# Performance work log

Hardware: AMD Instinct MI355X
Metric: run time of the kernel (lower is better)

Reference implementation:

```python
import jax, jax.numpy as jnp
import numpy as np

EMBED_DIM = 1024
NUM_HEADS = 16
D_K = EMBED_DIM // NUM_HEADS
GAMMA = 1.0


def setup_inputs() -> dict:
    key = jax.random.key(0)
    ks = jax.random.split(key, 5)
    B, N, E = 2, 2048, EMBED_DIM
    scale = 1.0 / np.sqrt(E)
    x = jax.random.normal(ks[0], (B, N, E), dtype=jnp.float32)
    Wq = jax.random.normal(ks[1], (E, E), dtype=jnp.float32) * scale
    Wk = jax.random.normal(ks[2], (E, E), dtype=jnp.float32) * scale
    Wv = jax.random.normal(ks[3], (E, E), dtype=jnp.float32) * scale
    Wo = jax.random.normal(ks[4], (E, E), dtype=jnp.float32) * scale
    mask = jnp.ones((B, N), dtype=jnp.int32)
    return {"x": x, "Wq": Wq, "Wk": Wk, "Wv": Wv, "Wo": Wo, "mask": mask}


def _split_heads(t):
    B, N, E = t.shape
    return t.reshape(B, N, NUM_HEADS, D_K).transpose(0, 2, 1, 3)  # [B,H,N,dk]


def reference(x, Wq, Wk, Wv, Wo, mask):
    B, N, E = x.shape
    # Linear layers (bias=False): y = x @ W.T
    q = _split_heads(x @ Wq.T)
    k = _split_heads(x @ Wk.T)
    v = _split_heads(x @ Wv.T)
    # Squared L2 distance via ||q||^2 + ||k||^2 - 2 q.k (same math as (q-k)^2.sum,
    # without materializing the [B,H,N,N,dk] diff tensor).
    q_sq = jnp.sum(q * q, axis=-1)  # [B,H,N]
    k_sq = jnp.sum(k * k, axis=-1)  # [B,H,N]
    qk = jnp.einsum('bhqd,bhkd->bhqk', q, k)
    sq_dist = jnp.maximum(q_sq[..., :, None] + k_sq[..., None, :] - 2.0 * qk, 0.0)
    similarity = jnp.exp(-GAMMA * sq_dist)  # [B,H,N,N]
    # mask.unsqueeze(1).unsqueeze(2): broadcast over heads and query dim
    mask_exp = mask[:, None, None, :]  # [B,1,1,N]
    similarity = jnp.where(mask_exp == 0, jnp.float32(-1e9), similarity)
    attn = jax.nn.softmax(similarity, axis=-1)
    # dropout p=0.0 (eval) -> identity
    out = jnp.einsum('bhqk,bhkd->bhqd', attn, v)
    out = out.transpose(0, 2, 1, 3).reshape(B, N, E)
    return out @ Wo.T
```

## Files before the change

kernel.cpp:

```cpp
#include <hip/hip_runtime.h>
#include <hip/hip_bf16.h>


using bf16x8 = __attribute__((ext_vector_type(8))) __bf16;
using f32x4  = __attribute__((ext_vector_type(4))) float;
using f32x16 = __attribute__((ext_vector_type(16))) float;

typedef const __attribute__((address_space(1))) void* gas_t;
typedef __attribute__((address_space(3))) void* las_t;

#define C_LOG2E 1.4426950408889634f
#define TWO_C   2.8853900817779268f
#define NEG_INV_4C (-0.17328679513998632f)

#if __has_builtin(__builtin_amdgcn_exp2f)
#define EXP2(x) __builtin_amdgcn_exp2f(x)
#else
#define EXP2(x) __expf((x) * 0.6931471805599453f)
#endif

static __device__ __forceinline__ unsigned short f2bf(float x) {
  union { float f; unsigned u; } c; c.f = x;
  unsigned u = c.u;
  u += 0x7fffu + ((u >> 16) & 1u);
  return (unsigned short)(u >> 16);
}
static __device__ __forceinline__ float bf2f(unsigned short b) {
  union { unsigned u; float f; } c; c.u = ((unsigned)b) << 16;
  return c.f;
}
static __device__ __forceinline__ unsigned cvt_pk_bf16(float lo, float hi) {
  unsigned r;
  asm("v_cvt_pk_bf16_f32 %0, %1, %2" : "=v"(r) : "v"(lo), "v"(hi));
  return r;
}
static __device__ __forceinline__ void permlane32_swap(unsigned &a, unsigned &b) {
#if __has_builtin(__builtin_amdgcn_permlane32_swap)
  auto r = __builtin_amdgcn_permlane32_swap(a, b, false, false);
  a = r[0]; b = r[1];
#else
  asm("v_permlane32_swap_b32 %0, %1" : "+v"(a), "+v"(b));
#endif
}

#define SYNC_VM(N)                                                           \
  do {                                                                       \
    asm volatile("s_waitcnt vmcnt(" #N ") lgkmcnt(0)\n\ts_barrier" ::: "memory"); \
    __builtin_amdgcn_sched_barrier(0);                                       \
  } while (0)

__global__ __launch_bounds__(256)
void cvt_all(const float* __restrict__ x,  const float* __restrict__ wq,
             const float* __restrict__ wk, const float* __restrict__ wv,
             const float* __restrict__ wo,
             unsigned short* __restrict__ xbf, unsigned short* __restrict__ Wbf) {
  const int idx = blockIdx.x * 256 + threadIdx.x;
  const float* src; unsigned short* dst; int off;
  if (idx < 1048576) { src = x; dst = xbf; off = idx; }
  else {
    const int r = idx - 1048576;
    const int w = r >> 18;
    off = r & 262143;
    src = (w == 0) ? wq : (w == 1) ? wk : (w == 2) ? wv : wo;
    dst = Wbf + (size_t)w * 1048576u;
  }
  const float4 v = ((const float4*)src)[off];
  ushort4 o;
  o.x = f2bf(v.x); o.y = f2bf(v.y); o.z = f2bf(v.z); o.w = f2bf(v.w);
  ((ushort4*)dst)[off] = o;
}

__global__ __launch_bounds__(256)
void gemm_bt(const unsigned short* __restrict__ A,
             const unsigned short* __restrict__ Bt,
             void* __restrict__ out0, int Kdim, int mode) {
  __shared__ unsigned short As[3][4096];
  __shared__ unsigned short Bs[3][4096];
  const int t  = threadIdx.x;
  const int m0 = blockIdx.x * 128;
  const int n0 = blockIdx.y * 128;
  const int srow = t >> 2;
  const int scol = (t & 3) * 8;
  const unsigned short* pA = A  + (size_t)(m0 + srow) * Kdim + scol;
  const unsigned short* pB = Bt + (size_t)(n0 + srow) * Kdim + scol;
  const size_t rowskip = (size_t)64 * Kdim;

  const int wave = t >> 6, lane = t & 63;
  const int wm = (wave >> 1) * 64, wn = (wave & 1) * 64;
  const int fr = lane & 15, fg = lane >> 4;
  const int aoff = (wm + fr) * 32 + fg * 8;
  const int boff = (wn + fr) * 32 + fg * 8;

  f32x4 acc[4][4];
#pragma unroll
  for (int mi = 0; mi < 4; ++mi)
#pragma unroll
    for (int ni = 0; ni < 4; ++ni)
      acc[mi][ni] = (f32x4){0.f, 0.f, 0.f, 0.f};

#define GSTAGE(bi, kk)                                                                                  \
  do {                                                                                                  \
    const int kc = (kk) * 32;                                                                           \
    __builtin_amdgcn_global_load_lds((gas_t)(const void*)(pA + kc),           (las_t)(void*)(As[bi] + t * 8),        16, 0, 0); \
    __builtin_amdgcn_global_load_lds((gas_t)(const void*)(pA + kc + rowskip), (las_t)(void*)(As[bi] + 2048 + t * 8), 16, 0, 0); \
    __builtin_amdgcn_global_load_lds((gas_t)(const void*)(pB + kc),           (las_t)(void*)(Bs[bi] + t * 8),        16, 0, 0); \
    __builtin_amdgcn_global_load_lds((gas_t)(const void*)(pB + kc + rowskip), (las_t)(void*)(Bs[bi] + 2048 + t * 8), 16, 0, 0); \
  } while (0)

  const int NK = Kdim >> 5;
  GSTAGE(0, 0);
  GSTAGE(1, 1);

  for (int ks = 0; ks < NK; ++ks) {
    const int cur = ks % 3;
    if (ks + 1 < NK) SYNC_VM(4); else SYNC_VM(0);
    if (ks + 2 < NK) GSTAGE((ks + 2) % 3, ks + 2);

    bf16x8 af[4], bfr[4];
#pragma unroll
    for (int mi = 0; mi < 4; ++mi) af[mi]  = *(const bf16x8*)(As[cur] + aoff + mi * 512);
#pragma unroll
    for (int ni = 0; ni < 4; ++ni) bfr[ni] = *(const bf16x8*)(Bs[cur] + boff + ni * 512);
#pragma unroll
    for (int mi = 0; mi < 4; ++mi)
#pragma unroll
      for (int ni = 0; ni < 4; ++ni)
        acc[mi][ni] = __builtin_amdgcn_mfma_f32_16x16x32_bf16(af[mi], bfr[ni], acc[mi][ni], 0, 0, 0);
  }
#undef GSTAGE

#pragma unroll
  for (int mi = 0; mi < 4; ++mi) {
    const int gm = m0 + wm + mi * 16 + fg * 4;
#pragma unroll
    for (int ni = 0; ni < 4; ++ni) {
      const int gn = n0 + wn + ni * 16 + fr;
      if (mode == 0) {
        unsigned short* outw = (unsigned short*)out0;
        const int z = gn >> 10, col = gn & 1023;
        if (z < 2) {
          const float sc = (z == 0) ? TWO_C : 1.0f;
          unsigned short* dst = outw + (size_t)z * 4194304u;
#pragma unroll
          for (int r = 0; r < 4; ++r)
            dst[(size_t)(gm + r) * 1024 + col] = f2bf(acc[mi][ni][r] * sc);
        } else {
          ushort4 o4;
          o4.x = f2bf(acc[mi][ni][0]); o4.y = f2bf(acc[mi][ni][1]);
          o4.z = f2bf(acc[mi][ni][2]); o4.w = f2bf(acc[mi][ni][3]);
          const int bb = gm >> 11, nn = gm & 2047;
          const int hh = col >> 6, dd = col & 63;
          unsigned short* vt = outw + (size_t)2 * 4194304u;
          *(ushort4*)(vt + ((size_t)((bb * 16 + hh) * 64 + dd)) * 2048 + nn) = o4;
        }
      } else {
        float* dst = (float*)out0;
#pragma unroll
        for (int r = 0; r < 4; ++r)
          dst[(size_t)(gm + r) * 1024 + gn] = acc[mi][ni][r];
      }
    }
  }
}

__global__ __launch_bounds__(256)
void rowsq_kernel(const unsigned short* __restrict__ Qbf,
                  const unsigned short* __restrict__ Kbf,
                  const int* __restrict__ mask,
                  float* __restrict__ qsqp, float* __restrict__ ksqp,
                  float* __restrict__ maskf,
                  float* __restrict__ FullVm,
                  float* __restrict__ den_base,
                  unsigned* __restrict__ kmax_bits) {
  const int tid = blockIdx.x * 256 + threadIdx.x;
  const int kpath = blockIdx.y;
  const unsigned short* src = (kpath == 0) ? Qbf : Kbf;
  const int bh = tid >> 11, n = tid & 2047;
  const int b = bh >> 4, h = bh & 15;
  const unsigned short* row = src + (size_t)(b * 2048 + n) * 1024 + h * 64;
  float s = 0.f;
#pragma unroll
  for (int c = 0; c < 64; c += 4) {
    ushort4 v = *(const ushort4*)(row + c);
    float f0 = bf2f(v.x), f1 = bf2f(v.y), f2 = bf2f(v.z), f3 = bf2f(v.w);
    s += f0 * f0 + f1 * f1 + f2 * f2 + f3 * f3;
  }
  if (kpath == 0) {
    qsqp[tid] = s * NEG_INV_4C;
    if (tid < 2048) FullVm[tid] = 0.f;
    if (tid < 32) kmax_bits[tid] = 0xFF800000u;
    if (tid < 2) den_base[tid] = 0.f;
  } else {
    ksqp[tid] = s * (-C_LOG2E);
    if (tid < 4096) maskf[tid] = (mask[tid] == 0) ? 0.f : 1.f;
  }
}

__global__ __launch_bounds__(256)
void prep2_kernel(const unsigned short* __restrict__ Vt,
                  const float* __restrict__ maskf,
                  const float* __restrict__ ksqp,
                  float* __restrict__ FullVm,
                  float* __restrict__ den_base,
                  unsigned* __restrict__ kmax_bits) {
  const int bh = blockIdx.x, c = blockIdx.y;
  const int b = bh >> 4;
  const int wave = threadIdx.x >> 6, lane = threadIdx.x & 63;
  const int k0 = c * 256;
  const float4 mv = *(const float4*)(maskf + b * 2048 + k0 + lane * 4);
#pragma unroll 4
  for (int dr = wave * 16; dr < wave * 16 + 16; ++dr) {
    const ushort4 v = *(const ushort4*)(Vt + ((size_t)bh * 64 + dr) * 2048 + k0 + lane * 4);
    float s = bf2f(v.x) * mv.x + bf2f(v.y) * mv.y + bf2f(v.z) * mv.z + bf2f(v.w) * mv.w;
#pragma unroll
    for (int off = 32; off >= 1; off >>= 1) s += __shfl_xor(s, off);
    if (lane == 0) atomicAdd(&FullVm[bh * 64 + dr], s);
  }
  if (wave == 0) {
    const float4 kq = *(const float4*)(ksqp + bh * 2048 + k0 + lane * 4);
    float mx = fmaxf(fmaxf(kq.x, kq.y), fmaxf(kq.z, kq.w));
#pragma unroll
    for (int off = 32; off >= 1; off >>= 1) mx = fmaxf(mx, __shfl_xor(mx, off));
    if (lane == 0) atomicMin(&kmax_bits[bh], __float_as_uint(mx));
  }
  if (wave == 1 && (bh & 15) == 0) {
    float s = mv.x + mv.y + mv.z + mv.w;
#pragma unroll
    for (int off = 32; off >= 1; off >>= 1) s += __shfl_xor(s, off);
    if (lane == 0) atomicAdd(&den_base[b], s);
  }
}

__global__ __launch_bounds__(256)
void attn_kernel(const unsigned short* __restrict__ Qbf,
                 const unsigned short* __restrict__ Kbf,
                 const unsigned short* __restrict__ Vt,
                 const float* __restrict__ qsqp,
                 const float* __restrict__ ksqp,
                 const float* __restrict__ maskf,
                 const float* __restrict__ FullVm,
                 const float* __restrict__ den_base,
                 const float* __restrict__ kmaxb,
                 unsigned short* __restrict__ Obf) {
  __shared__ unsigned short Ks[3][4096];

  const int bh = blockIdx.x;
  const int b = bh >> 4, h = bh & 15;
  const int t = threadIdx.x;
  const int wave = t >> 6, lane = t & 63;
  const int qg = wave >> 1, hf = wave & 1;
  const int li = lane & 31, hi = lane >> 5;
  const int q0 = blockIdx.y * 64 + qg * 32;
  const int qrow = q0 + li;

  const unsigned short* Qr = Qbf + (size_t)(b * 2048 + qrow) * 1024 + h * 64 + hi * 8;
  bf16x8 qf[4];
#pragma unroll
  for (int dblk = 0; dblk < 4; ++dblk) qf[dblk] = *(const bf16x8*)(Qr + dblk * 16);

  const float qsl = qsqp[bh * 2048 + qrow];
  const float thr = -14.0f - qsl - kmaxb[bh];

  const unsigned short* Kbase = Kbf + (size_t)b * 2048 * 1024 + h * 64;
  const unsigned short* VtB = Vt + (size_t)bh * 64 * 2048;

  const int p0 = t,        r0 = p0 >> 3, c0 = (p0 & 7) ^ (r0 & 7);
  const int p1 = 256 + t,  r1 = p1 >> 3, c1 = (p1 & 7) ^ (r1 & 7);

  f32x16 oa0, oa1;
#pragma unroll
  for (int r = 0; r < 16; ++r) { oa0[r] = 0.f; oa1[r] = 0.f; }
  float den = 0.f;

#define STAGE(bi, tj)                                                                               \
  do {                                                                                              \
    const int j0s = (tj) * 64;                                                                      \
    __builtin_amdgcn_global_load_lds((gas_t)(const void*)(Kbase + (size_t)(j0s + r0) * 1024 + c0 * 8), \
                                     (las_t)(void*)(Ks[bi] + p0 * 8), 16, 0, 0);                    \
    __builtin_amdgcn_global_load_lds((gas_t)(const void*)(Kbase + (size_t)(j0s + r1) * 1024 + c1 * 8), \
                                     (las_t)(void*)(Ks[bi] + p1 * 8), 16, 0, 0);                    \
  } while (0)

  STAGE(0, 0);
  STAGE(1, 1);

  const int jw = hf * 32;
  const int krow = jw + li;
  const int ksw = krow & 7;

  for (int tj = 0; tj < 32; ++tj) {
    const int cur = tj % 3;
    if (tj + 1 < 32) SYNC_VM(2); else SYNC_VM(0);
    if (tj + 2 < 32) STAGE((tj + 2) % 3, tj + 2);

    const unsigned short* Krow = Ks[cur] + krow * 64;
    f32x16 st;
#pragma unroll
    for (int r = 0; r < 16; ++r) st[r] = 0.f;
#pragma unroll
    for (int dblk = 0; dblk < 4; ++dblk) {
      const bf16x8 kf = *(const bf16x8*)(Krow + ((dblk * 2 + hi) ^ ksw) * 8);
      st = __builtin_amdgcn_mfma_f32_32x32x16_bf16(kf, qf[dblk], st, 0, 0, 0);
    }

    const float a0 = fmaxf(fmaxf(st[0], st[1]), st[2]);
    const float a1 = fmaxf(fmaxf(st[3], st[4]), st[5]);
    const float a2 = fmaxf(fmaxf(st[6], st[7]), st[8]);
    const float a3 = fmaxf(fmaxf(st[9], st[10]), st[11]);
    const float a4 = fmaxf(fmaxf(st[12], st[13]), st[14]);
    const float a5 = fmaxf(fmaxf(a0, a1), st[15]);
    const float a6 = fmaxf(fmaxf(a2, a3), a4);
    const float lmax = fmaxf(a5, a6);

    if (__any(lmax > thr)) {
      const int j0 = tj * 64 + jw;
      const float* ksb2 = ksqp + bh * 2048 + j0 + 4 * hi;
      const float* mfb2 = maskf + b * 2048 + j0 + 4 * hi;
      const float4 kq0 = *(const float4*)(ksb2);
      const float4 kq1 = *(const float4*)(ksb2 + 8);
      const float4 kq2 = *(const float4*)(ksb2 + 16);
      const float4 kq3 = *(const float4*)(ksb2 + 24);
      const float4 mf0 = *(const float4*)(mfb2);
      const float4 mf1 = *(const float4*)(mfb2 + 8);
      const float4 mf2 = *(const float4*)(mfb2 + 16);
      const float4 mf3 = *(const float4*)(mfb2 + 24);
      const float kqa[16] = {kq0.x, kq0.y, kq0.z, kq0.w, kq1.x, kq1.y, kq1.z, kq1.w,
                             kq2.x, kq2.y, kq2.z, kq2.w, kq3.x, kq3.y, kq3.z, kq3.w};
      const float mfa[16] = {mf0.x, mf0.y, mf0.z, mf0.w, mf1.x, mf1.y, mf1.z, mf1.w,
                             mf2.x, mf2.y, mf2.z, mf2.w, mf3.x, mf3.y, mf3.z, mf3.w};
      float dsv[16];
#pragma unroll
      for (int r = 0; r < 16; ++r) {
        const float z = __builtin_fminf(st[r] + qsl + kqa[r], 0.f);
        const float s = EXP2(z);
        float pl = __builtin_fmaf(s, 1.f / 120.f, 1.f / 24.f);
        pl = __builtin_fmaf(s, pl, 1.f / 6.f);
        pl = __builtin_fmaf(s, pl, 0.5f);
        pl = __builtin_fmaf(s, pl, 1.f);
        const float d_ = s * pl * mfa[r];
        dsv[r] = d_;
        den += d_;
      }

      unsigned u00 = cvt_pk_bf16(dsv[0],  dsv[1]);
      unsigned u01 = cvt_pk_bf16(dsv[2],  dsv[3]);
      unsigned u10 = cvt_pk_bf16(dsv[4],  dsv[5]);
      unsigned u11 = cvt_pk_bf16(dsv[6],  dsv[7]);
      unsigned u20 = cvt_pk_bf16(dsv[8],  dsv[9]);
      unsigned u21 = cvt_pk_bf16(dsv[10], dsv[11]);
      unsigned u30 = cvt_pk_bf16(dsv[12], dsv[13]);
      unsigned u31 = cvt_pk_bf16(dsv[14], dsv[15]);
      permlane32_swap(u00, u10);
      permlane32_swap(u01, u11);
      permlane32_swap(u20, u30);
      permlane32_swap(u21, u31);
      union { unsigned u[4]; bf16x8 v; } pf0, pf1;
      pf0.u[0] = u00; pf0.u[1] = u01; pf0.u[2] = u10; pf0.u[3] = u11;
      pf1.u[0] = u20; pf1.u[1] = u21; pf1.u[2] = u30; pf1.u[3] = u31;

#pragma unroll
      for (int dh = 0; dh < 2; ++dh) {
        const unsigned short* Vrow = VtB + (size_t)(dh * 32 + li) * 2048 + tj * 64;
        const bf16x8 vf0 = *(const bf16x8*)(Vrow + (hf * 4 + 0 + hi) * 8);
        const bf16x8 vf1 = *(const bf16x8*)(Vrow + (hf * 4 + 2 + hi) * 8);
        if (dh == 0) {
          oa0 = __builtin_amdgcn_mfma_f32_32x32x16_bf16(vf0, pf0.v, oa0, 0, 0, 0);
          oa0 = __builtin_amdgcn_mfma_f32_32x32x16_bf16(vf1, pf1.v, oa0, 0, 0, 0);
        } else {
          oa1 = __builtin_amdgcn_mfma_f32_32x32x16_bf16(vf0, pf0.v, oa1, 0, 0, 0);
          oa1 = __builtin_amdgcn_mfma_f32_32x32x16_bf16(vf1, pf1.v, oa1, 0, 0, 0);
        }
      }
    }
  }
#undef STAGE

  den += __shfl_xor(den, 32);

  __syncthreads();
  float* Obuf = (float*)&Ks[0][0];
  float* Dbuf = (float*)&Ks[0][0] + 4096;
  if (hf == 1) {
#pragma unroll
    for (int r = 0; r < 16; ++r) {
      Obuf[(qg * 32 + r) * 64 + lane]      = oa0[r];
      Obuf[(qg * 32 + 16 + r) * 64 + lane] = oa1[r];
    }
    Dbuf[qg * 64 + lane] = den;
  }
  __syncthreads();
  if (hf == 0) {
    const float inv = 1.f / (den_base[b] + den + Dbuf[qg * 64 + lane]);
    const float* fvm = FullVm + bh * 64;
    unsigned short* orow = Obf + (size_t)(b * 2048 + qrow) * 1024 + h * 64;
#pragma unroll
    for (int dh = 0; dh < 2; ++dh)
#pragma unroll
      for (int w = 0; w < 4; ++w) {
        float v0, v1, v2, v3;
        if (dh == 0) {
          v0 = oa0[4 * w];     v1 = oa0[4 * w + 1];
          v2 = oa0[4 * w + 2]; v3 = oa0[4 * w + 3];
        } else {
          v0 = oa1[4 * w];     v1 = oa1[4 * w + 1];
          v2 = oa1[4 * w + 2]; v3 = oa1[4 * w + 3];
        }
        const int sbase = (qg * 32 + dh * 16 + 4 * w) * 64 + lane;
        v0 += Obuf[sbase];       v1 += Obuf[sbase + 64];
        v2 += Obuf[sbase + 128]; v3 += Obuf[sbase + 192];
        const float4 fv = *(const float4*)(fvm + dh * 32 + w * 8 + hi * 4);
        ushort4 o4;
        o4.x = f2bf((v0 + fv.x) * inv);
        o4.y = f2bf((v1 + fv.y) * inv);
        o4.z = f2bf((v2 + fv.z) * inv);
        o4.w = f2bf((v3 + fv.w) * inv);
        *(ushort4*)(orow + dh * 32 + w * 8 + hi * 4) = o4;
      }
  }
}

extern "C" void kernel_launch(void* const* d_in, const int* in_sizes, int n_in,
                              void* d_out, int out_size, void* d_ws, size_t ws_size,
                              hipStream_t stream) {
  const float* x  = (const float*)d_in[0];
  const float* Wq = (const float*)d_in[1];
  const float* Wk = (const float*)d_in[2];
  const float* Wv = (const float*)d_in[3];
  const float* Wo = (const float*)d_in[4];
  const int* mask = (const int*)d_in[5];

  unsigned short* ws = (unsigned short*)d_ws;
  const size_t SZ = 4194304;
  unsigned short* xbf = ws;
  unsigned short* Wbf = ws + SZ;
  unsigned short* Qbf = ws + 2 * SZ;
  unsigned short* Kbf = ws + 3 * SZ;
  unsigned short* Vt  = ws + 4 * SZ;
  unsigned short* Obf = ws + 5 * SZ;
  float* qsqp = (float*)(ws + 6 * SZ);
  float* ksqp = qsqp + 65536;
  float* maskf = ksqp + 65536;
  float* FullVm = maskf + 4096;
  float* den_base = FullVm + 2048;
  float* kmaxb = den_base + 2;

  cvt_all<<<8192, 256, 0, stream>>>(x, Wq, Wk, Wv, Wo, xbf, Wbf);

  gemm_bt<<<dim3(32, 24), 256, 0, stream>>>(xbf, Wbf, Qbf, 1024, 0);

  rowsq_kernel<<<dim3(256, 2), 256, 0, stream>>>(Qbf, Kbf, mask, qsqp, ksqp, maskf,
                                                 FullVm, den_base, (unsigned*)kmaxb);

  prep2_kernel<<<dim3(32, 8), 256, 0, stream>>>(Vt, maskf, ksqp, FullVm, den_base,
                                                (unsigned*)kmaxb);

  attn_kernel<<<dim3(32, 32), 256, 0, stream>>>(Qbf, Kbf, Vt, qsqp, ksqp, maskf,
                                                FullVm, den_base, kmaxb, Obf);

  gemm_bt<<<dim3(32, 8), 256, 0, stream>>>(Obf, Wbf + 3145728, d_out, 1024, 1);
}
```

Measured before the change: 116.6 us.

## Double attention key tile per stage and swizzle GEMM LDS layout

The attention kernel now stages 128 keys per pipeline step instead of 64, so each wave computes two 32x32 score tiles per iteration. This halves the loop trip count and the barrier/wait overhead, and gives the scheduler two independent MFMA chains to interleave. The GEMM kernel also gets an XOR swizzle on LDS column chunks to reduce bank conflicts on fragment reads. In exchange, LDS use in attention doubles, which may reduce occupancy, and the larger unrolled body adds register pressure.

```diff
diff --git a/kernel.cpp b/kernel.cpp
--- a/kernel.cpp
+++ b/kernel.cpp
@@ -80,7 +80,7 @@
   const int m0 = blockIdx.x * 128;
   const int n0 = blockIdx.y * 128;
   const int srow = t >> 2;
-  const int scol = (t & 3) * 8;
+  const int scol = (((t & 3) ^ (srow & 3) ^ ((srow >> 2) & 3))) * 8;
   const unsigned short* pA = A  + (size_t)(m0 + srow) * Kdim + scol;
   const unsigned short* pB = Bt + (size_t)(n0 + srow) * Kdim + scol;
   const size_t rowskip = (size_t)64 * Kdim;
@@ -88,8 +88,9 @@
   const int wave = t >> 6, lane = t & 63;
   const int wm = (wave >> 1) * 64, wn = (wave & 1) * 64;
   const int fr = lane & 15, fg = lane >> 4;
-  const int aoff = (wm + fr) * 32 + fg * 8;
-  const int boff = (wn + fr) * 32 + fg * 8;
+  const int fswz = fg ^ (fr & 3) ^ ((fr >> 2) & 3);
+  const int aoff = (wm + fr) * 32 + fswz * 8;
+  const int boff = (wn + fr) * 32 + fswz * 8;
 
   f32x4 acc[4][4];
 #pragma unroll
@@ -242,7 +243,7 @@
                  const float* __restrict__ den_base,
                  const float* __restrict__ kmaxb,
                  unsigned short* __restrict__ Obf) {
-  __shared__ unsigned short Ks[3][4096];
+  __shared__ unsigned short Ks[3][8192];
 
   const int bh = blockIdx.x;
   const int b = bh >> 4, h = bh & 15;
@@ -264,8 +265,10 @@
   const unsigned short* Kbase = Kbf + (size_t)b * 2048 * 1024 + h * 64;
   const unsigned short* VtB = Vt + (size_t)bh * 64 * 2048;
 
-  const int p0 = t,        r0 = p0 >> 3, c0 = (p0 & 7) ^ (r0 & 7);
-  const int p1 = 256 + t,  r1 = p1 >> 3, c1 = (p1 & 7) ^ (r1 & 7);
+  const int p0 = t,       r0 = p0 >> 3, c0 = (p0 & 7) ^ (r0 & 7);
+  const int p1 = 256 + t, r1 = p1 >> 3, c1 = (p1 & 7) ^ (r1 & 7);
+  const int p2 = 512 + t, r2 = p2 >> 3, c2 = (p2 & 7) ^ (r2 & 7);
+  const int p3 = 768 + t, r3 = p3 >> 3, c3 = (p3 & 7) ^ (r3 & 7);
 
   f32x16 oa0, oa1;
 #pragma unroll
@@ -274,104 +277,114 @@
 
 #define STAGE(bi, tj)                                                                               \
   do {                                                                                              \
-    const int j0s = (tj) * 64;                                                                      \
+    const int j0s = (tj) * 128;                                                                     \
     __builtin_amdgcn_global_load_lds((gas_t)(const void*)(Kbase + (size_t)(j0s + r0) * 1024 + c0 * 8), \
                                      (las_t)(void*)(Ks[bi] + p0 * 8), 16, 0, 0);                    \
     __builtin_amdgcn_global_load_lds((gas_t)(const void*)(Kbase + (size_t)(j0s + r1) * 1024 + c1 * 8), \
                                      (las_t)(void*)(Ks[bi] + p1 * 8), 16, 0, 0);                    \
+    __builtin_amdgcn_global_load_lds((gas_t)(const void*)(Kbase + (size_t)(j0s + r2) * 1024 + c2 * 8), \
+                                     (las_t)(void*)(Ks[bi] + p2 * 8), 16, 0, 0);                    \
+    __builtin_amdgcn_global_load_lds((gas_t)(const void*)(Kbase + (size_t)(j0s + r3) * 1024 + c3 * 8), \
+                                     (las_t)(void*)(Ks[bi] + p3 * 8), 16, 0, 0);                    \
   } while (0)
 
   STAGE(0, 0);
   STAGE(1, 1);
 
-  const int jw = hf * 32;
-  const int krow = jw + li;
-  const int ksw = krow & 7;
-
-  for (int tj = 0; tj < 32; ++tj) {
-    const int cur = tj % 3;
-    if (tj + 1 < 32) SYNC_VM(2); else SYNC_VM(0);
-    if (tj + 2 < 32) STAGE((tj + 2) % 3, tj + 2);
-
-    const unsigned short* Krow = Ks[cur] + krow * 64;
-    f32x16 st;
-#pragma unroll
-    for (int r = 0; r < 16; ++r) st[r] = 0.f;
-#pragma unroll
-    for (int dblk = 0; dblk < 4; ++dblk) {
-      const bf16x8 kf = *(const bf16x8*)(Krow + ((dblk * 2 + hi) ^ ksw) * 8);
-      st = __builtin_amdgcn_mfma_f32_32x32x16_bf16(kf, qf[dblk], st, 0, 0, 0);
+  const int jw = hf * 64;
+  const int ksw = li & 7;
+
+  auto slow_path = [&](const f32x16& st, int j0s) {
+    const float* ksb2 = ksqp + bh * 2048 + j0s + 4 * hi;
+    const float* mfb2 = maskf + b * 2048 + j0s + 4 * hi;
+    const float4 kq0 = *(const float4*)(ksb2);
+    const float4 kq1 = *(const float4*)(ksb2 + 8);
+    const float4 kq2 = *(const float4*)(ksb2 + 16);
+    const float4 kq3 = *(const float4*)(ksb2 + 24);
+    const float4 mf0 = *(const float4*)(mfb2);
+    const float4 mf1 = *(const float4*)(mfb2 + 8);
+    const float4 mf2 = *(const float4*)(mfb2 + 16);
+    const float4 mf3 = *(const float4*)(mfb2 + 24);
+    const float kqa[16] = {kq0.x, kq0.y, kq0.z, kq0.w, kq1.x, kq1.y, kq1.z, kq1.w,
+                           kq2.x, kq2.y, kq2.z, kq2.w, kq3.x, kq3.y, kq3.z, kq3.w};
+    const float mfa[16] = {mf0.x, mf0.y, mf0.z, mf0.w, mf1.x, mf1.y, mf1.z, mf1.w,
+                           mf2.x, mf2.y, mf2.z, mf2.w, mf3.x, mf3.y, mf3.z, mf3.w};
+    float dsv[16];
+#pragma unroll
+    for (int r = 0; r < 16; ++r) {
+      const float z = __builtin_fminf(st[r] + qsl + kqa[r], 0.f);
+      const float s = EXP2(z);
+      float pl = __builtin_fmaf(s, 1.f / 120.f, 1.f / 24.f);
+      pl = __builtin_fmaf(s, pl, 1.f / 6.f);
+      pl = __builtin_fmaf(s, pl, 0.5f);
+      pl = __builtin_fmaf(s, pl, 1.f);
+      const float d_ = s * pl * mfa[r];
+      dsv[r] = d_;
+      den += d_;
     }
-
-    const float a0 = fmaxf(fmaxf(st[0], st[1]), st[2]);
-    const float a1 = fmaxf(fmaxf(st[3], st[4]), st[5]);
-    const float a2 = fmaxf(fmaxf(st[6], st[7]), st[8]);
-    const float a3 = fmaxf(fmaxf(st[9], st[10]), st[11]);
-    const float a4 = fmaxf(fmaxf(st[12], st[13]), st[14]);
-    const float a5 = fmaxf(fmaxf(a0, a1), st[15]);
-    const float a6 = fmaxf(fmaxf(a2, a3), a4);
-    const float lmax = fmaxf(a5, a6);
-
-    if (__any(lmax > thr)) {
-      const int j0 = tj * 64 + jw;
-      const float* ksb2 = ksqp + bh * 2048 + j0 + 4 * hi;
-      const float* mfb2 = maskf + b * 2048 + j0 + 4 * hi;
-      const float4 kq0 = *(const float4*)(ksb2);
-      const float4 kq1 = *(const float4*)(ksb2 + 8);
-      const float4 kq2 = *(const float4*)(ksb2 + 16);
-      const float4 kq3 = *(const float4*)(ksb2 + 24);
-      const float4 mf0 = *(const float4*)(mfb2);
-      const float4 mf1 = *(const float4*)(mfb2 + 8);
-      const float4 mf2 = *(const float4*)(mfb2 + 16);
-      const float4 mf3 = *(const float4*)(mfb2 + 24);
-      const float kqa[16] = {kq0.x, kq0.y, kq0.z, kq0.w, kq1.x, kq1.y, kq1.z, kq1.w,
-                             kq2.x, kq2.y, kq2.z, kq2.w, kq3.x, kq3.y, kq3.z, kq3.w};
-      const float mfa[16] = {mf0.x, mf0.y, mf0.z, mf0.w, mf1.x, mf1.y, mf1.z, mf1.w,
-                             mf2.x, mf2.y, mf2.z, mf2.w, mf3.x, mf3.y, mf3.z, mf3.w};
-      float dsv[16];
-#pragma unroll
-      for (int r = 0; r < 16; ++r) {
-        const float z = __builtin_fminf(st[r] + qsl + kqa[r], 0.f);
-        const float s = EXP2(z);
-        float pl = __builtin_fmaf(s, 1.f / 120.f, 1.f / 24.f);
-        pl = __builtin_fmaf(s, pl, 1.f / 6.f);
-        pl = __builtin_fmaf(s, pl, 0.5f);
-        pl = __builtin_fmaf(s, pl, 1.f);
-        const float d_ = s * pl * mfa[r];
-        dsv[r] = d_;
-        den += d_;
-      }
-
-      unsigned u00 = cvt_pk_bf16(dsv[0],  dsv[1]);
-      unsigned u01 = cvt_pk_bf16(dsv[2],  dsv[3]);
-      unsigned u10 = cvt_pk_bf16(dsv[4],  dsv[5]);
-      unsigned u11 = cvt_pk_bf16(dsv[6],  dsv[7]);
-      unsigned u20 = cvt_pk_bf16(dsv[8],  dsv[9]);
-      unsigned u21 = cvt_pk_bf16(dsv[10], dsv[11]);
-      unsigned u30 = cvt_pk_bf16(dsv[12], dsv[13]);
-      unsigned u31 = cvt_pk_bf16(dsv[14], dsv[15]);
-      permlane32_swap(u00, u10);
-      permlane32_swap(u01, u11);
-      permlane32_swap(u20, u30);
-      permlane32_swap(u21, u31);
-      union { unsigned u[4]; bf16x8 v; } pf0, pf1;
-      pf0.u[0] = u00; pf0.u[1] = u01; pf0.u[2] = u10; pf0.u[3] = u11;
-      pf1.u[0] = u20; pf1.u[1] = u21; pf1.u[2] = u30; pf1.u[3] = u31;
-
-#pragma unroll
-      for (int dh = 0; dh < 2; ++dh) {
-        const unsigned short* Vrow = VtB + (size_t)(dh * 32 + li) * 2048 + tj * 64;
-        const bf16x8 vf0 = *(const bf16x8*)(Vrow + (hf * 4 + 0 + hi) * 8);
-        const bf16x8 vf1 = *(const bf16x8*)(Vrow + (hf * 4 + 2 + hi) * 8);
-        if (dh == 0) {
-          oa0 = __builtin_amdgcn_mfma_f32_32x32x16_bf16(vf0, pf0.v, oa0, 0, 0, 0);
-          oa0 = __builtin_amdgcn_mfma_f32_32x32x16_bf16(vf1, pf1.v, oa0, 0, 0, 0);
-        } else {
-          oa1 = __builtin_amdgcn_mfma_f32_32x32x16_bf16(vf0, pf0.v, oa1, 0, 0, 0);
-          oa1 = __builtin_amdgcn_mfma_f32_32x32x16_bf16(vf1, pf1.v, oa1, 0, 0, 0);
-        }
+    unsigned u00 = cvt_pk_bf16(dsv[0],  dsv[1]);
+    unsigned u01 = cvt_pk_bf16(dsv[2],  dsv[3]);
+    unsigned u10 = cvt_pk_bf16(dsv[4],  dsv[5]);
+    unsigned u11 = cvt_pk_bf16(dsv[6],  dsv[7]);
+    unsigned u20 = cvt_pk_bf16(dsv[8],  dsv[9]);
+    unsigned u21 = cvt_pk_bf16(dsv[10], dsv[11]);
+    unsigned u30 = cvt_pk_bf16(dsv[12], dsv[13]);
+    unsigned u31 = cvt_pk_bf16(dsv[14], dsv[15]);
+    permlane32_swap(u00, u10);
+    permlane32_swap(u01, u11);
+    permlane32_swap(u20, u30);
+    permlane32_swap(u21, u31);
+    union { unsigned u[4]; bf16x8 v; } pf0, pf1;
+    pf0.u[0] = u00; pf0.u[1] = u01; pf0.u[2] = u10; pf0.u[3] = u11;
+    pf1.u[0] = u20; pf1.u[1] = u21; pf1.u[2] = u30; pf1.u[3] = u31;
+#pragma unroll
+    for (int dh = 0; dh < 2; ++dh) {
+      const unsigned short* Vrow = VtB + (size_t)(dh * 32 + li) * 2048 + j0s;
+      const bf16x8 vf0 = *(const bf16x8*)(Vrow + hi * 8);
+      const bf16x8 vf1 = *(const bf16x8*)(Vrow + 16 + hi * 8);
+      if (dh == 0) {
+        oa0 = __builtin_amdgcn_mfma_f32_32x32x16_bf16(vf0, pf0.v, oa0, 0, 0, 0);
+        oa0 = __builtin_amdgcn_mfma_f32_32x32x16_bf16(vf1, pf1.v, oa0, 0, 0, 0);
+      } else {
+        oa1 = __builtin_amdgcn_mfma_f32_32x32x16_bf16(vf0, pf0.v, oa1, 0, 0, 0);
+        oa1 = __builtin_amdgcn_mfma_f32_32x32x16_bf16(vf1, pf1.v, oa1, 0, 0, 0);
       }
     }
+  };
+
+  for (int tj = 0; tj < 16; ++tj) {
+    const int cur = tj % 3;
+    if (tj + 1 < 16) SYNC_VM(4); else SYNC_VM(0);
+    if (tj + 2 < 16) STAGE((tj + 2) % 3, tj + 2);
+
+    const unsigned short* Krow0 = Ks[cur] + (jw + li) * 64;
+    const unsigned short* Krow1 = Ks[cur] + (jw + 32 + li) * 64;
+    f32x16 st0, st1;
+#pragma unroll
+    for (int r = 0; r < 16; ++r) { st0[r] = 0.f; st1[r] = 0.f; }
+#pragma unroll
+    for (int dblk = 0; dblk < 4; ++dblk) {
+      const int ch = ((dblk * 2 + hi) ^ ksw) * 8;
+      const bf16x8 kf0 = *(const bf16x8*)(Krow0 + ch);
+      const bf16x8 kf1 = *(const bf16x8*)(Krow1 + ch);
+      st0 = __builtin_amdgcn_mfma_f32_32x32x16_bf16(kf0, qf[dblk], st0, 0, 0, 0);
+      st1 = __builtin_amdgcn_mfma_f32_32x32x16_bf16(kf1, qf[dblk], st1, 0, 0, 0);
+    }
+
+    const float a0 = fmaxf(fmaxf(st0[0], st0[1]), fmaxf(st0[2], st0[3]));
+    const float a1 = fmaxf(fmaxf(st0[4], st0[5]), fmaxf(st0[6], st0[7]));
+    const float a2 = fmaxf(fmaxf(st0[8], st0[9]), fmaxf(st0[10], st0[11]));
+    const float a3 = fmaxf(fmaxf(st0[12], st0[13]), fmaxf(st0[14], st0[15]));
+    const float lmax0 = fmaxf(fmaxf(a0, a1), fmaxf(a2, a3));
+    const float b0 = fmaxf(fmaxf(st1[0], st1[1]), fmaxf(st1[2], st1[3]));
+    const float b1 = fmaxf(fmaxf(st1[4], st1[5]), fmaxf(st1[6], st1[7]));
+    const float b2 = fmaxf(fmaxf(st1[8], st1[9]), fmaxf(st1[10], st1[11]));
+    const float b3 = fmaxf(fmaxf(st1[12], st1[13]), fmaxf(st1[14], st1[15]));
+    const float lmax1 = fmaxf(fmaxf(b0, b1), fmaxf(b2, b3));
+
+    const int j0 = tj * 128 + jw;
+    if (__any(lmax0 > thr)) slow_path(st0, j0);
+    if (__any(lmax1 > thr)) slow_path(st1, j0 + 32);
   }
 #undef STAGE
 
```

Measured after the change: 117.7 us. No clear change (+0.9%).

## Fuse row-norm computation into QKV GEMM epilogue and swizzle GEMM LDS layout

Applied to the files above, without the earlier changes.

Removes the separate rowsq kernel by computing per-head squared norms of Q and K inside the QKV GEMM epilogue, using shuffle reductions over the rounded bf16 values. Buffer initialisation moves into the conversion kernel, and mask conversion moves into the prep kernel, so there is one launch fewer and no second read of Q and K. It also adds an XOR swizzle to the GEMM shared-memory tile layout, aimed at reducing LDS bank conflicts. The cost is extra shuffles and stores in the GEMM epilogue.

```diff
diff --git a/kernel.cpp b/kernel.cpp
--- a/kernel.cpp
+++ b/kernel.cpp
@@ -53,8 +53,17 @@
 void cvt_all(const float* __restrict__ x,  const float* __restrict__ wq,
              const float* __restrict__ wk, const float* __restrict__ wv,
              const float* __restrict__ wo,
-             unsigned short* __restrict__ xbf, unsigned short* __restrict__ Wbf) {
+             unsigned short* __restrict__ xbf, unsigned short* __restrict__ Wbf,
+             float* __restrict__ FullVm, float* __restrict__ den_base,
+             unsigned* __restrict__ kmax_bits) {
   const int idx = blockIdx.x * 256 + threadIdx.x;
+  if (blockIdx.x == 0) {
+    const int tid = threadIdx.x;
+#pragma unroll
+    for (int i = 0; i < 8; ++i) FullVm[tid + i * 256] = 0.f;
+    if (tid < 32) kmax_bits[tid] = 0xFF800000u;
+    if (tid < 2) den_base[tid] = 0.f;
+  }
   const float* src; unsigned short* dst; int off;
   if (idx < 1048576) { src = x; dst = xbf; off = idx; }
   else {
@@ -73,14 +82,15 @@
 __global__ __launch_bounds__(256)
 void gemm_bt(const unsigned short* __restrict__ A,
              const unsigned short* __restrict__ Bt,
-             void* __restrict__ out0, int Kdim, int mode) {
+             void* __restrict__ out0, int Kdim, int mode,
+             float* __restrict__ qsqp, float* __restrict__ ksqp) {
   __shared__ unsigned short As[3][4096];
   __shared__ unsigned short Bs[3][4096];
   const int t  = threadIdx.x;
   const int m0 = blockIdx.x * 128;
   const int n0 = blockIdx.y * 128;
   const int srow = t >> 2;
-  const int scol = (t & 3) * 8;
+  const int scol = (((t & 3) ^ (srow & 3) ^ ((srow >> 2) & 3))) * 8;
   const unsigned short* pA = A  + (size_t)(m0 + srow) * Kdim + scol;
   const unsigned short* pB = Bt + (size_t)(n0 + srow) * Kdim + scol;
   const size_t rowskip = (size_t)64 * Kdim;
@@ -88,8 +98,9 @@
   const int wave = t >> 6, lane = t & 63;
   const int wm = (wave >> 1) * 64, wn = (wave & 1) * 64;
   const int fr = lane & 15, fg = lane >> 4;
-  const int aoff = (wm + fr) * 32 + fg * 8;
-  const int boff = (wn + fr) * 32 + fg * 8;
+  const int fswz = fg ^ (fr & 3) ^ ((fr >> 2) & 3);
+  const int aoff = (wm + fr) * 32 + fswz * 8;
+  const int boff = (wn + fr) * 32 + fswz * 8;
 
   f32x4 acc[4][4];
 #pragma unroll
@@ -129,89 +140,102 @@
   }
 #undef GSTAGE
 
-#pragma unroll
-  for (int mi = 0; mi < 4; ++mi) {
-    const int gm = m0 + wm + mi * 16 + fg * 4;
-#pragma unroll
-    for (int ni = 0; ni < 4; ++ni) {
-      const int gn = n0 + wn + ni * 16 + fr;
-      if (mode == 0) {
-        unsigned short* outw = (unsigned short*)out0;
-        const int z = gn >> 10, col = gn & 1023;
-        if (z < 2) {
-          const float sc = (z == 0) ? TWO_C : 1.0f;
-          unsigned short* dst = outw + (size_t)z * 4194304u;
-#pragma unroll
-          for (int r = 0; r < 4; ++r)
-            dst[(size_t)(gm + r) * 1024 + col] = f2bf(acc[mi][ni][r] * sc);
-        } else {
-          ushort4 o4;
-          o4.x = f2bf(acc[mi][ni][0]); o4.y = f2bf(acc[mi][ni][1]);
-          o4.z = f2bf(acc[mi][ni][2]); o4.w = f2bf(acc[mi][ni][3]);
-          const int bb = gm >> 11, nn = gm & 2047;
-          const int hh = col >> 6, dd = col & 63;
-          unsigned short* vt = outw + (size_t)2 * 4194304u;
-          *(ushort4*)(vt + ((size_t)((bb * 16 + hh) * 64 + dd)) * 2048 + nn) = o4;
-        }
-      } else {
-        float* dst = (float*)out0;
+  if (mode == 1) {
+    float* dst = (float*)out0;
+#pragma unroll
+    for (int mi = 0; mi < 4; ++mi) {
+      const int gm = m0 + wm + mi * 16 + fg * 4;
+#pragma unroll
+      for (int ni = 0; ni < 4; ++ni) {
+        const int gn = n0 + wn + ni * 16 + fr;
 #pragma unroll
         for (int r = 0; r < 4; ++r)
           dst[(size_t)(gm + r) * 1024 + gn] = acc[mi][ni][r];
       }
     }
+    return;
+  }
+  const int wavecol = n0 + wn;
+  const int zz = wavecol >> 10;
+  unsigned short* outw = (unsigned short*)out0;
+  if (zz < 2) {
+    const float sc = (zz == 0) ? TWO_C : 1.0f;
+    const float qscale = (zz == 0) ? NEG_INV_4C : -C_LOG2E;
+    unsigned short* dst = outw + (size_t)zz * 4194304u;
+    const int hh = (wavecol & 1023) >> 6;
+    float* dq = (zz == 0) ? qsqp : ksqp;
+#pragma unroll
+    for (int mi = 0; mi < 4; ++mi) {
+      const int gm = m0 + wm + mi * 16 + fg * 4;
+      float s0 = 0.f, s1 = 0.f, s2 = 0.f, s3 = 0.f;
+#pragma unroll
+      for (int ni = 0; ni < 4; ++ni) {
+        const int col = (wavecol + ni * 16 + fr) & 1023;
+        const unsigned short u0 = f2bf(acc[mi][ni][0] * sc);
+        const unsigned short u1 = f2bf(acc[mi][ni][1] * sc);
+        const unsigned short u2 = f2bf(acc[mi][ni][2] * sc);
+        const unsigned short u3 = f2bf(acc[mi][ni][3] * sc);
+        dst[(size_t)(gm + 0) * 1024 + col] = u0;
+        dst[(size_t)(gm + 1) * 1024 + col] = u1;
+        dst[(size_t)(gm + 2) * 1024 + col] = u2;
+        dst[(size_t)(gm + 3) * 1024 + col] = u3;
+        const float r0 = bf2f(u0), r1 = bf2f(u1), r2 = bf2f(u2), r3 = bf2f(u3);
+        s0 += r0 * r0; s1 += r1 * r1; s2 += r2 * r2; s3 += r3 * r3;
+      }
+#pragma unroll
+      for (int off2 = 1; off2 < 16; off2 <<= 1) {
+        s0 += __shfl_xor(s0, off2);
+        s1 += __shfl_xor(s1, off2);
+        s2 += __shfl_xor(s2, off2);
+        s3 += __shfl_xor(s3, off2);
+      }
+      if (fr == 0) {
+        const int bb = gm >> 11;
+        float4 o4;
+        o4.x = s0 * qscale; o4.y = s1 * qscale;
+        o4.z = s2 * qscale; o4.w = s3 * qscale;
+        *(float4*)(dq + (bb * 16 + hh) * 2048 + (gm & 2047)) = o4;
+      }
+    }
+  } else {
+#pragma unroll
+    for (int mi = 0; mi < 4; ++mi) {
+      const int gm = m0 + wm + mi * 16 + fg * 4;
+#pragma unroll
+      for (int ni = 0; ni < 4; ++ni) {
+        const int gn = n0 + wn + ni * 16 + fr;
+        const int col = gn & 1023;
+        ushort4 o4;
+        o4.x = f2bf(acc[mi][ni][0]); o4.y = f2bf(acc[mi][ni][1]);
+        o4.z = f2bf(acc[mi][ni][2]); o4.w = f2bf(acc[mi][ni][3]);
+        const int bb = gm >> 11, nn = gm & 2047;
+        const int hh = col >> 6, dd = col & 63;
+        unsigned short* vt = outw + (size_t)2 * 4194304u;
+        *(ushort4*)(vt + ((size_t)((bb * 16 + hh) * 64 + dd)) * 2048 + nn) = o4;
+      }
+    }
   }
 }
 
 __global__ __launch_bounds__(256)
-void rowsq_kernel(const unsigned short* __restrict__ Qbf,
-                  const unsigned short* __restrict__ Kbf,
-                  const int* __restrict__ mask,
-                  float* __restrict__ qsqp, float* __restrict__ ksqp,
-                  float* __restrict__ maskf,
-                  float* __restrict__ FullVm,
-                  float* __restrict__ den_base,
-                  unsigned* __restrict__ kmax_bits) {
-  const int tid = blockIdx.x * 256 + threadIdx.x;
-  const int kpath = blockIdx.y;
-  const unsigned short* src = (kpath == 0) ? Qbf : Kbf;
-  const int bh = tid >> 11, n = tid & 2047;
-  const int b = bh >> 4, h = bh & 15;
-  const unsigned short* row = src + (size_t)(b * 2048 + n) * 1024 + h * 64;
-  float s = 0.f;
-#pragma unroll
-  for (int c = 0; c < 64; c += 4) {
-    ushort4 v = *(const ushort4*)(row + c);
-    float f0 = bf2f(v.x), f1 = bf2f(v.y), f2 = bf2f(v.z), f3 = bf2f(v.w);
-    s += f0 * f0 + f1 * f1 + f2 * f2 + f3 * f3;
-  }
-  if (kpath == 0) {
-    qsqp[tid] = s * NEG_INV_4C;
-    if (tid < 2048) FullVm[tid] = 0.f;
-    if (tid < 32) kmax_bits[tid] = 0xFF800000u;
-    if (tid < 2) den_base[tid] = 0.f;
-  } else {
-    ksqp[tid] = s * (-C_LOG2E);
-    if (tid < 4096) maskf[tid] = (mask[tid] == 0) ? 0.f : 1.f;
-  }
-}
-
-__global__ __launch_bounds__(256)
-void prep2_kernel(const unsigned short* __restrict__ Vt,
-                  const float* __restrict__ maskf,
-                  const float* __restrict__ ksqp,
-                  float* __restrict__ FullVm,
-                  float* __restrict__ den_base,
-                  unsigned* __restrict__ kmax_bits) {
-  const int bh = blockIdx.x, c = blockIdx.y;
+void prep_kernel(const unsigned short* __restrict__ Vt,
+                 const int* __restrict__ mask,
+                 const float* __restrict__ ksqp,
+                 float* __restrict__ maskf,
+                 float* __restrict__ FullVm,
+                 float* __restrict__ den_base,
+                 unsigned* __restrict__ kmax_bits) {
+  const int bh = blockIdx.x >> 3, c = blockIdx.x & 7;
   const int b = bh >> 4;
   const int wave = threadIdx.x >> 6, lane = threadIdx.x & 63;
   const int k0 = c * 256;
-  const float4 mv = *(const float4*)(maskf + b * 2048 + k0 + lane * 4);
+  const int4 mi4 = *(const int4*)(mask + b * 2048 + k0 + lane * 4);
+  const float mvx = mi4.x ? 1.f : 0.f, mvy = mi4.y ? 1.f : 0.f;
+  const float mvz = mi4.z ? 1.f : 0.f, mvw = mi4.w ? 1.f : 0.f;
 #pragma unroll 4
   for (int dr = wave * 16; dr < wave * 16 + 16; ++dr) {
     const ushort4 v = *(const ushort4*)(Vt + ((size_t)bh * 64 + dr) * 2048 + k0 + lane * 4);
-    float s = bf2f(v.x) * mv.x + bf2f(v.y) * mv.y + bf2f(v.z) * mv.z + bf2f(v.w) * mv.w;
+    float s = bf2f(v.x) * mvx + bf2f(v.y) * mvy + bf2f(v.z) * mvz + bf2f(v.w) * mvw;
 #pragma unroll
     for (int off = 32; off >= 1; off >>= 1) s += __shfl_xor(s, off);
     if (lane == 0) atomicAdd(&FullVm[bh * 64 + dr], s);
@@ -224,7 +248,11 @@
     if (lane == 0) atomicMin(&kmax_bits[bh], __float_as_uint(mx));
   }
   if (wave == 1 && (bh & 15) == 0) {
-    float s = mv.x + mv.y + mv.z + mv.w;
+    float4 mf; mf.x = mvx; mf.y = mvy; mf.z = mvz; mf.w = mvw;
+    *(float4*)(maskf + b * 2048 + k0 + lane * 4) = mf;
+  }
+  if (wave == 2 && (bh & 15) == 0) {
+    float s = mvx + mvy + mvz + mvw;
 #pragma unroll
     for (int off = 32; off >= 1; off >>= 1) s += __shfl_xor(s, off);
     if (lane == 0) atomicAdd(&den_base[b], s);
@@ -444,18 +472,17 @@
   float* den_base = FullVm + 2048;
   float* kmaxb = den_base + 2;
 
-  cvt_all<<<8192, 256, 0, stream>>>(x, Wq, Wk, Wv, Wo, xbf, Wbf);
-
-  gemm_bt<<<dim3(32, 24), 256, 0, stream>>>(xbf, Wbf, Qbf, 1024, 0);
-
-  rowsq_kernel<<<dim3(256, 2), 256, 0, stream>>>(Qbf, Kbf, mask, qsqp, ksqp, maskf,
-                                                 FullVm, den_base, (unsigned*)kmaxb);
-
-  prep2_kernel<<<dim3(32, 8), 256, 0, stream>>>(Vt, maskf, ksqp, FullVm, den_base,
-                                                (unsigned*)kmaxb);
+  cvt_all<<<8192, 256, 0, stream>>>(x, Wq, Wk, Wv, Wo, xbf, Wbf,
+                                    FullVm, den_base, (unsigned*)kmaxb);
+
+  gemm_bt<<<dim3(32, 24), 256, 0, stream>>>(xbf, Wbf, Qbf, 1024, 0, qsqp, ksqp);
+
+  prep_kernel<<<256, 256, 0, stream>>>(Vt, mask, ksqp, maskf, FullVm, den_base,
+                                       (unsigned*)kmaxb);
 
   attn_kernel<<<dim3(32, 32), 256, 0, stream>>>(Qbf, Kbf, Vt, qsqp, ksqp, maskf,
                                                 FullVm, den_base, kmaxb, Obf);
 
-  gemm_bt<<<dim3(32, 8), 256, 0, stream>>>(Obf, Wbf + 3145728, d_out, 1024, 1);
-}
+  gemm_bt<<<dim3(32, 8), 256, 0, stream>>>(Obf, Wbf + 3145728, d_out, 1024, 1,
+                                           nullptr, nullptr);
+}
```

Result: faster. 112.1 us (-3.8%).
